# Kernel tuning notes

Measured on AMD Instinct MI355X. Metric: run time of the kernel, lower is better.

## Reference

```python
import jax, jax.numpy as jnp
import numpy as np


def setup_inputs() -> dict:
    key = jax.random.key(0)
    ks = jax.random.split(key, 5)
    B, H, W, dim = 2, 56, 56, 256
    heads, k = 8, 7
    s = 0.02
    return {
        "hidden_states": jax.random.normal(ks[0], (B, H, W, dim), jnp.float32),
        "wq": jax.random.normal(ks[1], (dim, dim), jnp.float32) * s,
        "bq": jnp.zeros((dim,), jnp.float32),
        "wk": jax.random.normal(ks[2], (dim, dim), jnp.float32) * s,
        "bk": jnp.zeros((dim,), jnp.float32),
        "wv": jax.random.normal(ks[3], (dim, dim), jnp.float32) * s,
        "bv": jnp.zeros((dim,), jnp.float32),
        "rpb": jax.random.normal(ks[4], (heads, 2 * k - 1, 2 * k - 1), jnp.float32) * s,
    }


def _window_start(L, k):
    # NATTEN window start for dilation=1: centered window, clamped to stay inside [0, L)
    ns = k // 2
    i = jnp.arange(L)
    return jnp.maximum(i - ns, 0) + jnp.where(i + ns >= L, L - i - ns - 1, 0)


def _neighborhood_attention(hidden_states, wq, bq, wk, bk, wv, bv, rpb):
    B, H, W, dim = hidden_states.shape
    heads = rpb.shape[0]
    k = (rpb.shape[1] + 1) // 2  # rpb is (heads, 2k-1, 2k-1)
    hd = dim // heads

    def proj(w, b):
        y = hidden_states @ w.T + b  # nn.Linear convention: x @ W^T + b
        return y.reshape(B, H, W, heads, hd).transpose(0, 3, 1, 2, 4)  # [B,h,H,W,d]

    q = proj(wq, bq) / jnp.sqrt(jnp.float32(hd))
    kl = proj(wk, bk)
    vl = proj(wv, bv)

    off = jnp.arange(k)
    ki = _window_start(H, k)[:, None] + off[None, :]  # [H,k] key row indices per query row
    kj = _window_start(W, k)[:, None] + off[None, :]  # [W,k] key col indices per query col

    def gather_nbhd(x):
        # x: [B,h,H,W,d] -> [B,h,H,W,k*k,d]
        g = x[:, :, ki[:, :, None, None], kj[None, None, :, :], :]  # [B,h,H,k,W,k,d]
        return g.transpose(0, 1, 2, 4, 3, 5, 6).reshape(B, heads, H, W, k * k, hd)

    kn = gather_nbhd(kl)
    vn = gather_nbhd(vl)

    # relative position bias index = (key_pos - query_pos) + (k - 1)
    pbi = ki - jnp.arange(H)[:, None] + (k - 1)  # [H,k]
    pbj = kj - jnp.arange(W)[:, None] + (k - 1)  # [W,k]
    bias = rpb[:, pbi[:, :, None, None], pbj[None, None, :, :]]  # [h,H,k,W,k]
    bias = bias.transpose(0, 1, 3, 2, 4).reshape(heads, H, W, k * k)

    scores = jnp.einsum('bnijd,bnijkd->bnijk', q, kn) + bias[None]
    probs = jax.nn.softmax(scores, axis=-1)  # dropout prob = 0.0 (eval)
    ctx = jnp.einsum('bnijk,bnijkd->bnijd', probs, vn)
    return ctx.transpose(0, 2, 3, 1, 4).reshape(B, H, W, dim)


def reference(hidden_states, wq, bq, wk, bk, wv, bv, rpb):
    return _neighborhood_attention(hidden_states, wq, bq, wk, bk, wv, bv, rpb)
```

## Files before the change

### kernel.cpp

```cpp
#include <hip/hip_runtime.h>
#include <hip/hip_bf16.h>

typedef __attribute__((ext_vector_type(8))) short bf16x8;
typedef __attribute__((ext_vector_type(4))) float f32x4;

#define NPIX 6272
#define HW 56
#define HEADS 8
#define HD 32
#define KW 7
#define DIM 256
#define GDIM 768
#define UK 112
#define UKP 128

__device__ inline short f2bf(float f) {
    __hip_bfloat16 h = __float2bfloat16(f);
    return *(short*)&h;
}
__device__ inline float bf2f(short u) {
    union { unsigned int i; float f; } x;
    x.i = ((unsigned int)(unsigned short)u) << 16;
    return x.f;
}
__device__ inline bf16x8 pack8(float4 f0, float4 f1) {
    bf16x8 v;
    v[0]=f2bf(f0.x); v[1]=f2bf(f0.y); v[2]=f2bf(f0.z); v[3]=f2bf(f0.w);
    v[4]=f2bf(f1.x); v[5]=f2bf(f1.y); v[6]=f2bf(f1.z); v[7]=f2bf(f1.w);
    return v;
}

__global__ __launch_bounds__(256, 2) void proj_kernel(
    const float* __restrict__ X,
    const float* __restrict__ Wq, const float* __restrict__ Wk, const float* __restrict__ Wv,
    const float* __restrict__ Bq, const float* __restrict__ Bk, const float* __restrict__ Bv,
    short* __restrict__ Y)
{
    __shared__ short Ash[64 * 256];
    __shared__ short Bsh[64 * 256];

    const int id   = blockIdx.x;
    const int flat = (id & 7) * 147 + (id >> 3);
    const int bx   = flat / 12;
    const int by   = flat - bx * 12;

    const int tid  = threadIdx.x;
    const int wave = tid >> 6;
    const int lane = tid & 63;
    const int l15  = lane & 15;
    const int hi   = lane >> 4;

    const int brow = bx * 64;
    const int bcol = by * 64;

    const int z = by >> 2;
    const float* Wb = (z == 0) ? Wq : (z == 1) ? Wk : Wv;
    const float* Bi = (z == 0) ? Bq : (z == 1) ? Bk : Bv;
    const float scale = (z == 0) ? 0.17677669529663687f : 1.0f;
    const int wcol0 = (bcol & 255);

    float4 af[16], wf[16];
    #pragma unroll
    for (int i = 0; i < 8; ++i) {
        const int slot = tid + i * 256;
        const int row  = slot >> 5;
        const int p    = slot & 31;
        const int ge   = ((p ^ (row & 7)) << 3);
        const float* asrc = X  + (size_t)(brow + row) * DIM + ge;
        const float* wsrc = Wb + (size_t)(wcol0 + row) * DIM + ge;
        af[2*i]   = *(const float4*)(asrc);
        af[2*i+1] = *(const float4*)(asrc + 4);
        wf[2*i]   = *(const float4*)(wsrc);
        wf[2*i+1] = *(const float4*)(wsrc + 4);
    }
    #pragma unroll
    for (int i = 0; i < 8; ++i) {
        const int slot = tid + i * 256;
        *(bf16x8*)(Ash + slot * 8) = pack8(af[2*i], af[2*i+1]);
        *(bf16x8*)(Bsh + slot * 8) = pack8(wf[2*i], wf[2*i+1]);
    }
    __syncthreads();

    f32x4 acc[4];
    #pragma unroll
    for (int c = 0; c < 4; ++c) acc[c] = (f32x4){0.f, 0.f, 0.f, 0.f};

    const int arow = wave * 16 + l15;
    #pragma unroll
    for (int kk = 0; kk < 8; ++kk) {
        const int ch = kk * 4 + hi;
        bf16x8 a = *(const bf16x8*)((char*)Ash + arow * 512 + ((ch ^ (arow & 7)) << 4));
        #pragma unroll
        for (int c = 0; c < 4; ++c) {
            const int bro = c * 16 + l15;
            bf16x8 b = *(const bf16x8*)((char*)Bsh + bro * 512 + ((ch ^ (bro & 7)) << 4));
            acc[c] = __builtin_amdgcn_mfma_f32_16x16x32_bf16(a, b, acc[c], 0, 0, 0);
        }
    }

    #pragma unroll
    for (int c = 0; c < 4; ++c) {
        const int ocol = bcol + c * 16 + l15;
        const float bvv = Bi[ocol & 255];
        #pragma unroll
        for (int r = 0; r < 4; ++r) {
            const int row = brow + wave * 16 + hi * 4 + r;
            Y[(size_t)row * GDIM + ocol] = f2bf((acc[c][r] + bvv) * scale);
        }
    }
}

__global__ __launch_bounds__(256, 4) void nattn_kernel(
    const short* __restrict__ Yg,
    const float* __restrict__ rpb,
    float* __restrict__ out)
{
    __shared__ short VshT[128 * UKP];
    __shared__ __align__(16) short rpbs[8 * 169];

    const int id   = blockIdx.x;
    const int flat = (id & 7) * 98 + (id >> 3);
    const int bz   = flat / 392;
    int rem        = flat - bz * 392;
    const int ip   = rem / 14;
    rem           -= ip * 14;
    const int hg   = rem / 7;
    const int jt   = rem - hg * 7;

    const int tid  = threadIdx.x;
    const int wv   = tid >> 6;
    const int lane = tid & 63;
    const int l15  = lane & 15;
    const int hi   = lane >> 4;

    const int i0 = 2 * ip;
    const int j0 = jt * 8;
    const int r0 = min(max(i0 - 3, 0), HW - KW);
    const int c0 = min(max(j0 - 3, 0), HW - KW);

    const int h = hg * 4 + wv;

    const int k2   = tid & 63;
    const int dblk = tid >> 6;
    const int keyL = 2 * k2, keyR = 2 * k2 + 1;
    const int aL = keyL / 14, cL = keyL - aL * 14;
    const int aR = keyR / 14, cR = keyR - aR * 14;
    const int giL = min(r0 + aL, HW - 1), gjL = min(c0 + cL, HW - 1);
    const int giR = min(r0 + aR, HW - 1), gjR = min(c0 + cR, HW - 1);
    const short* srcL = Yg + (size_t)((bz * HW + giL) * HW + gjL) * GDIM + 512 + hg * 128 + dblk * 32;
    const short* srcR = Yg + (size_t)((bz * HW + giR) * HW + gjR) * GDIM + 512 + hg * 128 + dblk * 32;
    bf16x8 vL[4], vR[4];
    #pragma unroll
    for (int m = 0; m < 4; ++m) {
        vL[m] = (keyL < UK) ? *(const bf16x8*)(srcL + m * 8) : (bf16x8){0,0,0,0,0,0,0,0};
        vR[m] = (keyR < UK) ? *(const bf16x8*)(srcR + m * 8) : (bf16x8){0,0,0,0,0,0,0,0};
    }

    const int qpix = (bz * HW + i0 + (l15 >> 3)) * HW + j0 + (l15 & 7);
    bf16x8 aq = *(const bf16x8*)(Yg + (size_t)qpix * GDIM + h * HD + hi * 8);

    const float4* rpb4 = (const float4*)rpb;
    float4 rv0 = rpb4[tid];
    float4 rv1 = (tid < 338 - 256) ? rpb4[tid + 256] : (float4){0.f,0.f,0.f,0.f};

    #pragma unroll
    for (int m = 0; m < 4; ++m) {
        #pragma unroll
        for (int e = 0; e < 8; ++e) {
            const int d = dblk * 32 + m * 8 + e;
            const int w = ((int)(unsigned short)vL[m][e]) | ((int)vR[m][e] << 16);
            *(int*)((char*)VshT + d * 256 + ((4 * k2) ^ (e << 4))) = w;
        }
    }
    *(short4*)(&rpbs[tid * 4]) = make_short4(f2bf(rv0.x), f2bf(rv0.y), f2bf(rv0.z), f2bf(rv0.w));
    if (tid < 338 - 256)
        *(short4*)(&rpbs[(tid + 256) * 4]) = make_short4(f2bf(rv1.x), f2bf(rv1.y), f2bf(rv1.z), f2bf(rv1.w));
    __syncthreads();

    const int iv = i0 + (l15 >> 3);
    const int jv = j0 + (l15 & 7);
    const int siv = min(max(iv - 3, 0), HW - KW);
    const int sjv = min(max(jv - 3, 0), HW - KW);
    const int bb  = (r0 - iv + 6) * 13 + (c0 - jv + 6);
    const int uai = siv - r0;
    const int ucj = sjv - c0;
    const f32x4 zf = {0.f, 0.f, 0.f, 0.f};

    f32x4 sacc[7];
    {
        bf16x8 kb[7];
        #pragma unroll
        for (int t = 0; t < 7; ++t) {
            const int key = t * 16 + l15;
            const int a = key / 14, c = key - a * 14;
            const int gi = min(r0 + a, HW - 1), gj = min(c0 + c, HW - 1);
            kb[t] = *(const bf16x8*)(Yg + (size_t)((bz * HW + gi) * HW + gj) * GDIM +
                                     256 + h * HD + hi * 8);
        }
        #pragma unroll
        for (int t = 0; t < 7; ++t)
            sacc[t] = __builtin_amdgcn_mfma_f32_16x16x32_bf16(kb[t], aq, zf, 0, 0, 0);
    }

    const short* rbh = rpbs + h * 169;
    float sc[7][4];
    #pragma unroll
    for (int t = 0; t < 7; ++t) {
        #pragma unroll
        for (int r = 0; r < 4; ++r) {
            const int key = t * 16 + (hi << 2) + r;
            const int a = key / 14, c = key - a * 14;
            const bool ok = ((unsigned)(a - uai) <= 6u) & ((unsigned)(c - ucj) <= 6u);
            const float s = sacc[t][r] + bf2f(rbh[bb + a * 13 + c]);
            sc[t][r] = ok ? s : -1e30f;
        }
    }

    float m = sc[0][0];
    #pragma unroll
    for (int t = 0; t < 7; ++t)
        #pragma unroll
        for (int r = 0; r < 4; ++r) m = fmaxf(m, sc[t][r]);
    m = fmaxf(m, __shfl_xor(m, 16));
    m = fmaxf(m, __shfl_xor(m, 32));

    float sm = 0.f;
    unsigned long long pk[7];
    #pragma unroll
    for (int t = 0; t < 7; ++t) {
        float e0 = __expf(sc[t][0] - m), e1 = __expf(sc[t][1] - m);
        float e2 = __expf(sc[t][2] - m), e3 = __expf(sc[t][3] - m);
        sm += (e0 + e1) + (e2 + e3);
        const unsigned u0 = (unsigned)(unsigned short)f2bf(e0) |
                            ((unsigned)(unsigned short)f2bf(e1) << 16);
        const unsigned u1 = (unsigned)(unsigned short)f2bf(e2) |
                            ((unsigned)(unsigned short)f2bf(e3) << 16);
        pk[t] = (unsigned long long)u0 | ((unsigned long long)u1 << 32);
    }
    sm += __shfl_xor(sm, 16);
    sm += __shfl_xor(sm, 32);

    const int s0 = l15 + ((hi & 1) << 5);
    const bool hiSel = (hi >> 1) & 1;
    const int d0 = wv * 32 + l15;
    f32x4 o0 = zf, o1 = zf;
    #pragma unroll
    for (int kk = 0; kk < 4; ++kk) {
        unsigned long long a0 = __shfl(pk[2 * kk], s0, 64);
        unsigned long long b0 = __shfl(pk[2 * kk], s0 + 16, 64);
        unsigned long long a1 = 0ULL, b1 = 0ULL;
        if (2 * kk + 1 < 7) {
            a1 = __shfl(pk[2 * kk + 1], s0, 64);
            b1 = __shfl(pk[2 * kk + 1], s0 + 16, 64);
        }
        bf16x8 pa;
        ((unsigned long long*)&pa)[0] = hiSel ? a1 : a0;
        ((unsigned long long*)&pa)[1] = hiSel ? b1 : b0;

        const int koff = (kk * 64 + hi * 16) ^ ((l15 & 7) << 4);
        bf16x8 va0 = *(const bf16x8*)((char*)VshT + d0 * 256 + koff);
        bf16x8 va1 = *(const bf16x8*)((char*)VshT + (d0 + 16) * 256 + koff);
        o0 = __builtin_amdgcn_mfma_f32_16x16x32_bf16(va0, pa, o0, 0, 0, 0);
        o1 = __builtin_amdgcn_mfma_f32_16x16x32_bf16(va1, pa, o1, 0, 0, 0);
    }

    const float inv = 1.f / sm;
    float4 w0, w1;
    w0.x = o0[0] * inv; w0.y = o0[1] * inv; w0.z = o0[2] * inv; w0.w = o0[3] * inv;
    w1.x = o1[0] * inv; w1.y = o1[1] * inv; w1.z = o1[2] * inv; w1.w = o1[3] * inv;
    float* orow = out + (size_t)qpix * DIM + h * HD + hi * 4;
    *(float4*)(orow)      = w0;
    *(float4*)(orow + 16) = w1;
}

extern "C" void kernel_launch(void* const* d_in, const int* in_sizes, int n_in,
                              void* d_out, int out_size, void* d_ws, size_t ws_size,
                              hipStream_t stream) {
    const float* hs = (const float*)d_in[0];
    const float* wq = (const float*)d_in[1];
    const float* bq = (const float*)d_in[2];
    const float* wk = (const float*)d_in[3];
    const float* bk = (const float*)d_in[4];
    const float* wv = (const float*)d_in[5];
    const float* bv = (const float*)d_in[6];
    const float* rpb = (const float*)d_in[7];

    short* Y = (short*)d_ws;

    proj_kernel<<<1176, 256, 0, stream>>>(hs, wq, wk, wv, bq, bk, bv, Y);

    nattn_kernel<<<784, 256, 0, stream>>>(Y, rpb, (float*)d_out);
}
```

Before: 27.46 us.

## Reuse A tile across three output column tiles per projection block

Each projection block now loads and converts its 64-row slice of X to bf16 once, then loops over three 64-column weight tiles, so the grid shrinks from 1176 to 392 blocks. The goal is to cut redundant global reads and fp32-to-bf16 conversion of the activation tile. The cost is less parallelism (392 blocks on a 256-CU GPU, with occupancy limited by 64KB LDS), serialized weight loads with extra barriers inside each block, and no overlap between the weight fetch and the MFMA work.

```diff
diff --git a/kernel.cpp b/kernel.cpp
--- a/kernel.cpp
+++ b/kernel.cpp
@@ -40,9 +40,9 @@
     __shared__ short Bsh[64 * 256];
 
     const int id   = blockIdx.x;
-    const int flat = (id & 7) * 147 + (id >> 3);
-    const int bx   = flat / 12;
-    const int by   = flat - bx * 12;
+    const int flat = (id & 7) * 49 + (id >> 3);
+    const int bx   = flat >> 2;
+    const int bg   = flat & 3;
 
     const int tid  = threadIdx.x;
     const int wave = tid >> 6;
@@ -51,62 +51,85 @@
     const int hi   = lane >> 4;
 
     const int brow = bx * 64;
-    const int bcol = by * 64;
-
-    const int z = by >> 2;
-    const float* Wb = (z == 0) ? Wq : (z == 1) ? Wk : Wv;
-    const float* Bi = (z == 0) ? Bq : (z == 1) ? Bk : Bv;
-    const float scale = (z == 0) ? 0.17677669529663687f : 1.0f;
-    const int wcol0 = (bcol & 255);
-
-    float4 af[16], wf[16];
-    #pragma unroll
-    for (int i = 0; i < 8; ++i) {
-        const int slot = tid + i * 256;
-        const int row  = slot >> 5;
-        const int p    = slot & 31;
-        const int ge   = ((p ^ (row & 7)) << 3);
-        const float* asrc = X  + (size_t)(brow + row) * DIM + ge;
-        const float* wsrc = Wb + (size_t)(wcol0 + row) * DIM + ge;
-        af[2*i]   = *(const float4*)(asrc);
-        af[2*i+1] = *(const float4*)(asrc + 4);
-        wf[2*i]   = *(const float4*)(wsrc);
-        wf[2*i+1] = *(const float4*)(wsrc + 4);
-    }
-    #pragma unroll
-    for (int i = 0; i < 8; ++i) {
-        const int slot = tid + i * 256;
-        *(bf16x8*)(Ash + slot * 8) = pack8(af[2*i], af[2*i+1]);
-        *(bf16x8*)(Bsh + slot * 8) = pack8(wf[2*i], wf[2*i+1]);
-    }
-    __syncthreads();
-
-    f32x4 acc[4];
-    #pragma unroll
-    for (int c = 0; c < 4; ++c) acc[c] = (f32x4){0.f, 0.f, 0.f, 0.f};
+
+    {
+        float4 af[16];
+        #pragma unroll
+        for (int i = 0; i < 8; ++i) {
+            const int slot = tid + i * 256;
+            const int row  = slot >> 5;
+            const int p    = slot & 31;
+            const int ge   = ((p ^ (row & 7)) << 3);
+            const float* asrc = X + (size_t)(brow + row) * DIM + ge;
+            af[2*i]   = *(const float4*)(asrc);
+            af[2*i+1] = *(const float4*)(asrc + 4);
+        }
+        #pragma unroll
+        for (int i = 0; i < 8; ++i) {
+            const int slot = tid + i * 256;
+            *(bf16x8*)(Ash + slot * 8) = pack8(af[2*i], af[2*i+1]);
+        }
+    }
 
     const int arow = wave * 16 + l15;
-    #pragma unroll
-    for (int kk = 0; kk < 8; ++kk) {
-        const int ch = kk * 4 + hi;
-        bf16x8 a = *(const bf16x8*)((char*)Ash + arow * 512 + ((ch ^ (arow & 7)) << 4));
+
+    #pragma unroll
+    for (int cg = 0; cg < 3; ++cg) {
+        const int by   = bg * 3 + cg;
+        const int bcol = by * 64;
+        const int z    = by >> 2;
+        const float* Wb = (z == 0) ? Wq : (z == 1) ? Wk : Wv;
+        const float* Bi = (z == 0) ? Bq : (z == 1) ? Bk : Bv;
+        const float scale = (z == 0) ? 0.17677669529663687f : 1.0f;
+        const int w0 = (by & 3) * 64;
+
+        {
+            float4 wf[16];
+            #pragma unroll
+            for (int i = 0; i < 8; ++i) {
+                const int slot = tid + i * 256;
+                const int row  = slot >> 5;
+                const int p    = slot & 31;
+                const int ge   = ((p ^ (row & 7)) << 3);
+                const float* wsrc = Wb + (size_t)(w0 + row) * DIM + ge;
+                wf[2*i]   = *(const float4*)(wsrc);
+                wf[2*i+1] = *(const float4*)(wsrc + 4);
+            }
+            #pragma unroll
+            for (int i = 0; i < 8; ++i) {
+                const int slot = tid + i * 256;
+                *(bf16x8*)(Bsh + slot * 8) = pack8(wf[2*i], wf[2*i+1]);
+            }
+        }
+        __syncthreads();
+
+        f32x4 acc[4];
+        #pragma unroll
+        for (int c = 0; c < 4; ++c) acc[c] = (f32x4){0.f, 0.f, 0.f, 0.f};
+
+        #pragma unroll
+        for (int kk = 0; kk < 8; ++kk) {
+            const int ch = kk * 4 + hi;
+            bf16x8 a = *(const bf16x8*)((char*)Ash + arow * 512 + ((ch ^ (arow & 7)) << 4));
+            #pragma unroll
+            for (int c = 0; c < 4; ++c) {
+                const int bro = c * 16 + l15;
+                bf16x8 b = *(const bf16x8*)((char*)Bsh + bro * 512 + ((ch ^ (bro & 7)) << 4));
+                acc[c] = __builtin_amdgcn_mfma_f32_16x16x32_bf16(a, b, acc[c], 0, 0, 0);
+            }
+        }
+
         #pragma unroll
         for (int c = 0; c < 4; ++c) {
-            const int bro = c * 16 + l15;
-            bf16x8 b = *(const bf16x8*)((char*)Bsh + bro * 512 + ((ch ^ (bro & 7)) << 4));
-            acc[c] = __builtin_amdgcn_mfma_f32_16x16x32_bf16(a, b, acc[c], 0, 0, 0);
-        }
-    }
-
-    #pragma unroll
-    for (int c = 0; c < 4; ++c) {
-        const int ocol = bcol + c * 16 + l15;
-        const float bvv = Bi[ocol & 255];
-        #pragma unroll
-        for (int r = 0; r < 4; ++r) {
-            const int row = brow + wave * 16 + hi * 4 + r;
-            Y[(size_t)row * GDIM + ocol] = f2bf((acc[c][r] + bvv) * scale);
-        }
+            const int ocol = bcol + c * 16 + l15;
+            const float bvv = Bi[ocol & 255];
+            #pragma unroll
+            for (int r = 0; r < 4; ++r) {
+                const int row = brow + wave * 16 + hi * 4 + r;
+                Y[(size_t)row * GDIM + ocol] = f2bf((acc[c][r] + bvv) * scale);
+            }
+        }
+        if (cg < 2) __syncthreads();
     }
 }
 
@@ -287,7 +310,7 @@
 
     short* Y = (short*)d_ws;
 
-    proj_kernel<<<1176, 256, 0, stream>>>(hs, wq, wk, wv, bq, bk, bv, Y);
+    proj_kernel<<<392, 256, 0, stream>>>(hs, wq, wk, wv, bq, bk, bv, Y);
 
     nattn_kernel<<<784, 256, 0, stream>>>(Y, rpb, (float*)d_out);
 }
```

Result: faster. 26.89 us, median of 2 (-2.1%).
